# Performance work log

Measured on AMD Instinct MI355X. Metric: run time of the kernel, lower is better.

The kernel has to match this reference:

```python
import jax, jax.numpy as jnp
import numpy as np

N = 8192      # num nodes (fea.shape[0])
IN = 512      # in_features (fea.shape[1])
H = 64        # nhidden
DEG = 32      # avg degree
E = N * DEG   # num edges


def setup_inputs() -> dict:
    key = jax.random.key(0)
    k1, k2, k3 = jax.random.split(key, 3)
    x = jax.random.normal(k1, (N, IN), dtype=jnp.float32)
    # glorot-uniform-scaled params (stored as [in, out] for x @ W)
    W = jax.random.uniform(k2, (IN, H), jnp.float32, -1.0, 1.0) * np.sqrt(6.0 / (IN + H))
    a = jax.random.uniform(k3, (2 * H, 1), jnp.float32, -1.0, 1.0) * np.sqrt(6.0 / (2 * H + 1))
    # structured edge list: no self-loops, no duplicate edges (matches nonzero of a
    # zero-diagonal adjacency; indexed-assignment scatter then has unique targets)
    src = jnp.repeat(jnp.arange(N, dtype=jnp.int32), DEG)
    offs = jnp.tile(jnp.arange(1, DEG + 1, dtype=jnp.int32), N)
    dst = (src + offs) % N
    edge_index = jnp.stack([src, dst])  # [2, E]
    return {"x": x, "W": W, "a": a, "edge_index": edge_index}


def reference(x, W, a, edge_index):
    src, dst = edge_index[0], edge_index[1]
    n = x.shape[0]
    h = a.shape[0] // 2
    Wx = x @ W                                   # [N, H]
    # cat(fea1, fea2) @ a  ==  fea1 @ a[:h] + fea2 @ a[h:]
    e = (Wx @ a[:h])[src, 0] + (Wx @ a[h:])[dst, 0]   # [E]
    coef = jnp.exp(jax.nn.leaky_relu(e, negative_slope=0.1))
    # dense scatter into NxN adjacency (faithful to original)
    A = jnp.zeros((n, n), dtype=x.dtype).at[src, dst].set(coef)
    s1 = A.sum(axis=1)
    # rows with zero sum get a 1 on the diagonal (diag is 0 there, so add == set)
    diag = jnp.arange(n)
    A = A.at[diag, diag].add(jnp.where(s1 == 0, jnp.float32(1.0), jnp.float32(0.0)))
    # (A.t() / A.sum(1)).t()  ==  row-normalize
    return A / A.sum(axis=1, keepdims=True)
```

## Files before the change

### kernel.cpp

```cpp
#include <hip/hip_runtime.h>

#define N_NODES 8192
#define IN_F    512
#define NH      64
#define RB      512

typedef float v4f __attribute__((ext_vector_type(4)));

__global__ void k_prep(const float* __restrict__ W, const float* __restrict__ a,
                       float* __restrict__ wa1, float* __restrict__ wa2) {
    int tid = blockIdx.x * blockDim.x + threadIdx.x;
    if (tid < IN_F) {
        const float* wrow = W + tid * NH;
        float d1 = 0.f, d2 = 0.f;
#pragma unroll
        for (int k = 0; k < NH; ++k) {
            float w = wrow[k];
            d1 += w * a[k];
            d2 += w * a[NH + k];
        }
        wa1[tid] = d1;
        wa2[tid] = d2;
    }
}

__global__ void k_scores(const float* __restrict__ x, const float* __restrict__ wa1,
                         const float* __restrict__ wa2, float* __restrict__ s1,
                         float* __restrict__ s2) {
    int gid  = blockIdx.x * blockDim.x + threadIdx.x;
    int node = gid >> 6;
    int lane = threadIdx.x & 63;
    if (node >= N_NODES) return;
    const float4* xr = (const float4*)(x + (size_t)node * IN_F);
    const float4* w1 = (const float4*)wa1;
    const float4* w2 = (const float4*)wa2;
    float d1 = 0.f, d2 = 0.f;
#pragma unroll
    for (int i = 0; i < 2; ++i) {
        int idx = lane + 64 * i;
        float4 xv = xr[idx];
        float4 a1 = w1[idx];
        float4 a2 = w2[idx];
        d1 += xv.x * a1.x + xv.y * a1.y + xv.z * a1.z + xv.w * a1.w;
        d2 += xv.x * a2.x + xv.y * a2.y + xv.z * a2.z + xv.w * a2.w;
    }
#pragma unroll
    for (int off = 32; off > 0; off >>= 1) {
        d1 += __shfl_xor(d1, off, 64);
        d2 += __shfl_xor(d2, off, 64);
    }
    if (lane == 0) { s1[node] = d1; s2[node] = d2; }
}

__global__ __launch_bounds__(RB)
void k_row(const int* __restrict__ src, const int* __restrict__ dst,
           const float* __restrict__ s1, const float* __restrict__ s2,
           float* __restrict__ out, int deg) {
    const int row = blockIdx.x;
    const int tid = threadIdx.x;
    __shared__ float rowbuf[N_NODES];
    __shared__ float csum[RB];

    v4f* rb4 = (v4f*)rowbuf;
    const v4f z = {0.f, 0.f, 0.f, 0.f};
#pragma unroll
    for (int i = 0; i < (N_NODES / 4) / RB; ++i)
        rb4[tid + RB * i] = z;

    float c = 0.f;
    int col = -1;
    if (tid < deg) {
        int e  = row * deg + tid;
        int sv = src[e], dv = dst[e];
        float ev = s1[sv] + s2[dv];
        float l  = ev > 0.f ? ev : 0.1f * ev;
        c = expf(l);
        if (sv == row) col = dv;
    }
    csum[tid] = c;
    __syncthreads();
    if (col >= 0) rowbuf[col] = c;

    for (int s = RB / 2; s > 0; s >>= 1) {
        if (tid < s) csum[tid] += csum[tid + s];
        __syncthreads();
    }
    const float rs = csum[0];
    if (tid == 0 && rs == 0.f) rowbuf[row] = 1.0f;
    __syncthreads();
    const float inv = (rs == 0.f) ? 1.0f : 1.0f / rs;

    v4f* orow4 = (v4f*)(out + (size_t)row * N_NODES);
#pragma unroll
    for (int i = 0; i < (N_NODES / 4) / RB; ++i) {
        int idx = tid + RB * i;
        v4f v = rb4[idx];
        v *= inv;
        __builtin_nontemporal_store(v, &orow4[idx]);
    }
}

extern "C" void kernel_launch(void* const* d_in, const int* in_sizes, int n_in,
                              void* d_out, int out_size, void* d_ws, size_t ws_size,
                              hipStream_t stream) {
    const float* x  = (const float*)d_in[0];
    const float* W  = (const float*)d_in[1];
    const float* a  = (const float*)d_in[2];
    const int*   ei = (const int*)d_in[3];
    const int E = in_sizes[3] / 2;
    const int deg = E / N_NODES;
    const int* src = ei;
    const int* dst = ei + E;

    float* ws  = (float*)d_ws;
    float* wa1 = ws;
    float* wa2 = wa1 + IN_F;
    float* s1  = wa2 + IN_F;
    float* s2  = s1 + N_NODES;

    float* out = (float*)d_out;

    k_prep<<<(IN_F + 255) / 256, 256, 0, stream>>>(W, a, wa1, wa2);
    k_scores<<<(N_NODES * 64) / 256, 256, 0, stream>>>(x, wa1, wa2, s1, s2);
    k_row<<<N_NODES, RB, 0, stream>>>(src, dst, s1, s2, out, deg);
}
```

Baseline: 286.7 us.

## Fuse output zero-fill into score kernel and scatter sparse row values

The bulk zero-fill of the dense NxN output moves into the score kernel as a grid-stride nontemporal store. A new one-wave-per-row kernel computes the row sum with shuffles and scatters only the nonzero normalized coefficients. This removes the per-row shared-memory staging buffer and block-wide reduction. In exchange it adds a second pass over edges that recomputes exp, and the scatter writes are uncoalesced and must follow the fill. It also assumes edges are grouped by source row with exactly deg edges per row, as the earlier code did.

New measurement: 304.1 us. 6.1% more time.

```diff
diff --git a/kernel.cpp b/kernel.cpp
--- a/kernel.cpp
+++ b/kernel.cpp
@@ -3,7 +3,6 @@
 #define N_NODES 8192
 #define IN_F    512
 #define NH      64
-#define RB      512
 
 typedef float v4f __attribute__((ext_vector_type(4)));
 
@@ -24,13 +23,13 @@
     }
 }
 
-__global__ void k_scores(const float* __restrict__ x, const float* __restrict__ wa1,
-                         const float* __restrict__ wa2, float* __restrict__ s1,
-                         float* __restrict__ s2) {
-    int gid  = blockIdx.x * blockDim.x + threadIdx.x;
-    int node = gid >> 6;
-    int lane = threadIdx.x & 63;
-    if (node >= N_NODES) return;
+__global__ void k_scores_fill(const float* __restrict__ x, const float* __restrict__ wa1,
+                              const float* __restrict__ wa2, float* __restrict__ s1,
+                              float* __restrict__ s2, float* __restrict__ out) {
+    const int gid  = blockIdx.x * blockDim.x + threadIdx.x;
+    const int node = gid >> 6;
+    const int lane = threadIdx.x & 63;
+
     const float4* xr = (const float4*)(x + (size_t)node * IN_F);
     const float4* w1 = (const float4*)wa1;
     const float4* w2 = (const float4*)wa2;
@@ -50,53 +49,48 @@
         d2 += __shfl_xor(d2, off, 64);
     }
     if (lane == 0) { s1[node] = d1; s2[node] = d2; }
+
+    const v4f z = {0.f, 0.f, 0.f, 0.f};
+    v4f* o4 = (v4f*)out;
+    const size_t n4     = (size_t)N_NODES * N_NODES / 4;
+    const size_t stride = (size_t)gridDim.x * blockDim.x;
+    for (size_t i = (size_t)gid; i < n4; i += stride)
+        __builtin_nontemporal_store(z, &o4[i]);
 }
 
-__global__ __launch_bounds__(RB)
-void k_row(const int* __restrict__ src, const int* __restrict__ dst,
-           const float* __restrict__ s1, const float* __restrict__ s2,
-           float* __restrict__ out, int deg) {
-    const int row = blockIdx.x;
-    const int tid = threadIdx.x;
-    __shared__ float rowbuf[N_NODES];
-    __shared__ float csum[RB];
+__global__ void k_scatter(const int* __restrict__ src, const int* __restrict__ dst,
+                          const float* __restrict__ s1, const float* __restrict__ s2,
+                          float* __restrict__ out, int deg) {
+    const int gid  = blockIdx.x * blockDim.x + threadIdx.x;
+    const int row  = gid >> 6;
+    const int lane = threadIdx.x & 63;
 
-    v4f* rb4 = (v4f*)rowbuf;
-    const v4f z = {0.f, 0.f, 0.f, 0.f};
-#pragma unroll
-    for (int i = 0; i < (N_NODES / 4) / RB; ++i)
-        rb4[tid + RB * i] = z;
-
-    float c = 0.f;
-    int col = -1;
-    if (tid < deg) {
-        int e  = row * deg + tid;
+    const long base = (long)row * deg;
+    float sum = 0.f;
+    for (int t = lane; t < deg; t += 64) {
+        long e = base + t;
         int sv = src[e], dv = dst[e];
         float ev = s1[sv] + s2[dv];
         float l  = ev > 0.f ? ev : 0.1f * ev;
-        c = expf(l);
-        if (sv == row) col = dv;
+        sum += expf(l);
     }
-    csum[tid] = c;
-    __syncthreads();
-    if (col >= 0) rowbuf[col] = c;
+#pragma unroll
+    for (int off = 32; off > 0; off >>= 1)
+        sum += __shfl_xor(sum, off, 64);
+    const float rs = sum;
 
-    for (int s = RB / 2; s > 0; s >>= 1) {
-        if (tid < s) csum[tid] += csum[tid + s];
-        __syncthreads();
+    if (rs == 0.f) {
+        if (lane == 0) out[(size_t)row * N_NODES + row] = 1.0f;
+        return;
     }
-    const float rs = csum[0];
-    if (tid == 0 && rs == 0.f) rowbuf[row] = 1.0f;
-    __syncthreads();
-    const float inv = (rs == 0.f) ? 1.0f : 1.0f / rs;
-
-    v4f* orow4 = (v4f*)(out + (size_t)row * N_NODES);
-#pragma unroll
-    for (int i = 0; i < (N_NODES / 4) / RB; ++i) {
-        int idx = tid + RB * i;
-        v4f v = rb4[idx];
-        v *= inv;
-        __builtin_nontemporal_store(v, &orow4[idx]);
+    const float inv = 1.0f / rs;
+    for (int t = lane; t < deg; t += 64) {
+        long e = base + t;
+        int sv = src[e], dv = dst[e];
+        if (sv != row) continue;
+        float ev = s1[sv] + s2[dv];
+        float l  = ev > 0.f ? ev : 0.1f * ev;
+        out[(size_t)row * N_NODES + dv] = expf(l) * inv;
     }
 }
 
@@ -121,6 +115,6 @@
     float* out = (float*)d_out;
 
     k_prep<<<(IN_F + 255) / 256, 256, 0, stream>>>(W, a, wa1, wa2);
-    k_scores<<<(N_NODES * 64) / 256, 256, 0, stream>>>(x, wa1, wa2, s1, s2);
-    k_row<<<N_NODES, RB, 0, stream>>>(src, dst, s1, s2, out, deg);
+    k_scores_fill<<<(N_NODES * 64) / 256, 256, 0, stream>>>(x, wa1, wa2, s1, s2, out);
+    k_scatter<<<(N_NODES * 64) / 256, 256, 0, stream>>>(src, dst, s1, s2, out, deg);
 }
```
